# Kernel tuning notes

Measured on AMD Instinct MI355X. Metric: run time of the kernel, lower is better.

Reference implementation:

```python
import jax, jax.numpy as jnp
import numpy as np

B, C, H, W = 8, 256, 64, 64
CI = 128  # inter_channels = in_channels // reduction

def _conv1x1(x, w, b):
    # x: [b, c, h, w], w: [o, c], b: [o]
    return jnp.einsum('bchw,oc->bohw', x, w) + b[None, :, None, None]

def setup_inputs() -> dict:
    key = jax.random.key(0)
    ks = jax.random.split(key, 5)
    s_in = 1.0 / np.sqrt(C)
    s_ci = 1.0 / np.sqrt(CI)
    return {
        'x': jax.random.normal(ks[0], (B, C, H, W), jnp.float32),
        'w_g': jax.random.normal(ks[1], (CI, C), jnp.float32) * s_in,
        'b_g': jnp.zeros((CI,), jnp.float32),
        'w_theta': jax.random.normal(ks[2], (CI, C), jnp.float32) * s_in,
        'b_theta': jnp.zeros((CI,), jnp.float32),
        'w_phi': jax.random.normal(ks[3], (CI, C), jnp.float32) * s_in,
        'b_phi': jnp.zeros((CI,), jnp.float32),
        'w_out': jax.random.normal(ks[4], (C, CI), jnp.float32) * s_ci,
        'b_out': jnp.zeros((C,), jnp.float32),
    }

def reference(x, w_g, b_g, w_theta, b_theta, w_phi, b_phi, w_out, b_out):
    n, c, h, w = x.shape
    N = h * w
    g_x = _conv1x1(x, w_g, b_g).reshape(n, CI, N).transpose(0, 2, 1)        # [b, N, ci]
    theta_x = _conv1x1(x, w_theta, b_theta).reshape(n, CI, N).transpose(0, 2, 1)  # [b, N, ci]
    phi_x = _conv1x1(x, w_phi, b_phi).reshape(n, CI, N)                     # [b, ci, N]
    pw = jnp.einsum('bnc,bcm->bnm', theta_x, phi_x)                         # [b, N, N]
    # Faithful to source: divides by ci**(-0.5) == multiplies by sqrt(ci)
    pw = pw / (jnp.asarray(CI, x.dtype) ** -0.5)
    pw = jax.nn.softmax(pw, axis=-1)
    y = jnp.einsum('bnm,bmc->bnc', pw, g_x)                                 # [b, N, ci]
    y = y.transpose(0, 2, 1).reshape(n, CI, h, w)
    return x + _conv1x1(y, w_out, b_out)
```

## Files before the change

### kernel.cpp

```cpp
#include <hip/hip_runtime.h>
#include <hip/hip_bf16.h>
#include <stdint.h>
#include <stddef.h>


typedef __bf16 bf16;
typedef __attribute__((ext_vector_type(8))) __bf16 bf16x8;
typedef __attribute__((ext_vector_type(4))) __bf16 bf16x4;
typedef __attribute__((ext_vector_type(4))) float  f32x4;
typedef __attribute__((ext_vector_type(4))) int    i32x4;

#define MFMA16(a, b, c) __builtin_amdgcn_mfma_f32_16x16x32_bf16((a), (b), (c), 0, 0, 0)

constexpr int NB  = 8;
constexpr int NC  = 256;
constexpr int NN  = 4096;
constexpr int NCI = 128;
constexpr size_t NEL = (size_t)NB * NN * NCI;
constexpr int PBATCH = NN * NCI;

#define QSCALE (11.313708498984761f * 1.4426950408889634f)


__global__ __launch_bounds__(256) void k_proj(
    const float* __restrict__ x,
    const float* __restrict__ wt, const float* __restrict__ bt,
    const float* __restrict__ wp, const float* __restrict__ bp,
    const float* __restrict__ wg, const float* __restrict__ bg,
    bf16* __restrict__ qh, bf16* __restrict__ ql,
    bf16* __restrict__ kh, bf16* __restrict__ kl,
    bf16* __restrict__ vv)
{
    const int nt  = blockIdx.x;
    const int pj  = blockIdx.y;
    const int b   = blockIdx.z;
    const int tid = threadIdx.x;
    const int wv  = tid >> 6;
    const int ln  = tid & 63;
    const int lg  = ln >> 4;
    const int lq  = ln & 15;

    const float* W;
    const float* bias;
    if (pj == 0)      { W = wt; bias = bt; }
    else if (pj == 1) { W = wp; bias = bp; }
    else              { W = wg; bias = bg; }
    const bool split = (pj != 2);

    __shared__ char lds[49152];
    char* Ah = lds;
    char* Al = lds + 8192;
    char* Wh = lds + 16384;
    char* Wl = lds + 32768;

    f32x4 acc[8];
#pragma unroll
    for (int j = 0; j < 8; ++j) acc[j] = f32x4{0.f, 0.f, 0.f, 0.f};

    const int n0 = nt * 64;

    for (int c0 = 0; c0 < NC; c0 += 64) {
        __syncthreads();
#pragma unroll
        for (int p = 0; p < 4; ++p) {
            int cc = p * 16 + (tid >> 4);
            int nn = (tid & 15) * 4;
            f32x4 xv = *(const f32x4*)(x + ((size_t)b * NC + (c0 + cc)) * NN + n0 + nn);
#pragma unroll
            for (int e = 0; e < 4; ++e) {
                float f = xv[e];
                bf16 hh = (bf16)f;
                int row = nn + e;
                int off = (row * 128 + cc * 2) ^ ((row & 7) << 4);
                *(bf16*)(Ah + off) = hh;
                *(bf16*)(Al + off) = (bf16)(f - (float)hh);
            }
        }
#pragma unroll
        for (int p = 0; p < 8; ++p) {
            int i  = p * 16 + (tid >> 4);
            int c4 = (tid & 15) * 4;
            f32x4 w4 = *(const f32x4*)(W + (size_t)i * NC + c0 + c4);
            bf16x4 hv, lv;
#pragma unroll
            for (int e = 0; e < 4; ++e) {
                bf16 hh = (bf16)w4[e];
                hv[e] = hh;
                lv[e] = (bf16)(w4[e] - (float)hh);
            }
            int off = (i * 128 + c4 * 2) ^ ((i & 7) << 4);
            *(bf16x4*)(Wh + off) = hv;
            if (split) *(bf16x4*)(Wl + off) = lv;
        }
        __syncthreads();
#pragma unroll
        for (int kk = 0; kk < 2; ++kk) {
            int row  = wv * 16 + lq;
            int koff = kk * 64 + lg * 16;
            int aoff = (row * 128 + koff) ^ ((row & 7) << 4);
            bf16x8 ah = *(const bf16x8*)(Ah + aoff);
            bf16x8 al = *(const bf16x8*)(Al + aoff);
#pragma unroll
            for (int j = 0; j < 8; ++j) {
                int ir   = j * 16 + lq;
                int woff = (ir * 128 + koff) ^ ((ir & 7) << 4);
                bf16x8 bh = *(const bf16x8*)(Wh + woff);
                acc[j] = MFMA16(ah, bh, acc[j]);
                if (split) {
                    bf16x8 bl = *(const bf16x8*)(Wl + woff);
                    acc[j] = MFMA16(ah, bl, acc[j]);
                    acc[j] = MFMA16(al, bh, acc[j]);
                }
            }
        }
    }

    if (pj == 2) {
        __syncthreads();
        char* T = lds;
#pragma unroll
        for (int j = 0; j < 8; ++j) {
            int i = j * 16 + lq;
            float bv2 = bias[i];
#pragma unroll
            for (int r = 0; r < 4; ++r) {
                int nl = wv * 16 + lg * 4 + r;
                int off = (i * 128 + nl * 2) ^ ((i & 7) << 4);
                *(bf16*)(T + off) = (bf16)(acc[j][r] + bv2);
            }
        }
        __syncthreads();
#pragma unroll
        for (int p = 0; p < 4; ++p) {
            int i  = p * 32 + (tid >> 3);
            int sl = tid & 7;
            i32x4 tv = *(const i32x4*)(T + ((i * 128 + sl * 16) ^ ((i & 7) << 4)));
            size_t off = (size_t)b * PBATCH
                       + (size_t)((((nt * 8 + (i >> 4)) * 2 + (sl >> 2)) * 64
                                   + (sl & 3) * 16 + (i & 15)) * 8);
            *(i32x4*)(vv + off) = tv;
        }
    } else {
        const float sc = (pj == 0) ? QSCALE : 1.0f;
#pragma unroll
        for (int j = 0; j < 8; ++j) {
            int i = j * 16 + lq;
            float bv2 = bias[i];
#pragma unroll
            for (int r = 0; r < 4; ++r) {
                int q = n0 + wv * 16 + lg * 4 + r;
                size_t off = ((size_t)b * NN + q) * NCI + i;
                float val = (acc[j][r] + bv2) * sc;
                bf16 hh = (bf16)val;
                bf16 ll = (bf16)(val - (float)hh);
                if (pj == 0) { qh[off] = hh; ql[off] = ll; }
                else         { kh[off] = hh; kl[off] = ll; }
            }
        }
    }
}

__global__ __launch_bounds__(256, 2) void k_attn(
    const bf16* __restrict__ qh, const bf16* __restrict__ ql,
    const bf16* __restrict__ kh, const bf16* __restrict__ kl,
    const bf16* __restrict__ vf, bf16* __restrict__ y)
{
    const int bid = blockIdx.x;
    const int b   = bid & 7;
    const int qt  = bid >> 3;
    const int tid = threadIdx.x;
    const int wv  = tid >> 6;
    const int ln  = tid & 63;
    const int lg  = ln >> 4;
    const int lq  = ln & 15;
    const int n0  = qt * 64;

    __shared__ __attribute__((aligned(16))) char lds[40960];
    char* KH = lds;
    char* KL = lds + 16384;
    char* P  = lds + 32768 + wv * 2048;

    bf16x8 qhf[4], qlf[4];
    {
        int qrow = n0 + wv * 16 + lq;
        const bf16* bh = qh + ((size_t)b * NN + qrow) * NCI;
        const bf16* bl = ql + ((size_t)b * NN + qrow) * NCI;
#pragma unroll
        for (int kk = 0; kk < 4; ++kk) {
            int d0 = kk * 32 + lg * 8;
            qhf[kk] = *(const bf16x8*)(bh + d0);
            qlf[kk] = *(const bf16x8*)(bl + d0);
        }
    }

    f32x4 o[8];
#pragma unroll
    for (int j = 0; j < 8; ++j) o[j] = f32x4{0.f, 0.f, 0.f, 0.f};
    float mrun = -1e30f, lrun = 0.f;

    const bf16* vb = vf + (size_t)b * PBATCH + (size_t)ln * 8;

    for (int m0 = 0; m0 < NN; m0 += 64) {
        __syncthreads();
#pragma unroll
        for (int p = 0; p < 4; ++p) {
            int mm = p * 16 + (tid >> 4);
            int sl = tid & 15;
            size_t g = ((size_t)b * NN + m0 + mm) * NCI + sl * 8;
            int off = (mm * 256 + sl * 16) ^ ((mm & 7) << 4);
            *(i32x4*)(KH + off) = *(const i32x4*)(kh + g);
            *(i32x4*)(KL + off) = *(const i32x4*)(kl + g);
        }
        __syncthreads();

        bf16x8 bv[8][2];
        {
            const bf16* vp = vb + (size_t)(m0 >> 6) * 8192;
#pragma unroll
            for (int j = 0; j < 8; ++j) {
                bv[j][0] = *(const bf16x8*)(vp + (j * 2 + 0) * 512);
                bv[j][1] = *(const bf16x8*)(vp + (j * 2 + 1) * 512);
            }
        }

        f32x4 s[4];
        __builtin_amdgcn_s_setprio(1);
#pragma unroll
        for (int jm = 0; jm < 4; ++jm) {
            s[jm] = f32x4{0.f, 0.f, 0.f, 0.f};
            const int mrow = jm * 16 + lq;
            const int sw = (mrow & 7) << 4;
#pragma unroll
            for (int kk = 0; kk < 4; ++kk) {
                int aoff = (mrow * 256 + kk * 64 + lg * 16) ^ sw;
                bf16x8 ah = *(const bf16x8*)(KH + aoff);
                bf16x8 al = *(const bf16x8*)(KL + aoff);
                s[jm] = MFMA16(ah, qhf[kk], s[jm]);
                s[jm] = MFMA16(al, qhf[kk], s[jm]);
                s[jm] = MFMA16(ah, qlf[kk], s[jm]);
            }
        }
        __builtin_amdgcn_s_setprio(0);

        float tm = s[0][0];
#pragma unroll
        for (int jm = 0; jm < 4; ++jm)
#pragma unroll
            for (int r = 0; r < 4; ++r) tm = fmaxf(tm, s[jm][r]);
        tm = fmaxf(tm, __shfl_xor(tm, 16));
        tm = fmaxf(tm, __shfl_xor(tm, 32));

        if (__any(tm > mrun + 8.f)) {
            float mnew = fmaxf(mrun, tm);
            float alpha = exp2f(mrun - mnew);
            mrun = mnew;
            lrun *= alpha;
            float av[4];
#pragma unroll
            for (int r = 0; r < 4; ++r) av[r] = __shfl(alpha, lg * 4 + r);
#pragma unroll
            for (int j = 0; j < 8; ++j)
#pragma unroll
                for (int r = 0; r < 4; ++r) o[j][r] *= av[r];
        }

        float psum = 0.f;
#pragma unroll
        for (int jm = 0; jm < 4; ++jm) {
            bf16x4 pk;
#pragma unroll
            for (int r = 0; r < 4; ++r) {
                float e2 = exp2f(s[jm][r] - mrun);
                psum += e2;
                pk[r] = (bf16)e2;
            }
            int off = (lq * 128 + (jm * 16 + lg * 4) * 2) ^ ((lq & 7) << 4);
            *(bf16x4*)(P + off) = pk;
        }
        psum += __shfl_xor(psum, 16);
        psum += __shfl_xor(psum, 32);
        lrun += psum;

        bf16x8 pa[2];
#pragma unroll
        for (int tt = 0; tt < 2; ++tt)
            pa[tt] = *(const bf16x8*)(P + ((lq * 128 + tt * 64 + lg * 16) ^ ((lq & 7) << 4)));
        __builtin_amdgcn_s_setprio(1);
#pragma unroll
        for (int j = 0; j < 8; ++j) {
            o[j] = MFMA16(pa[0], bv[j][0], o[j]);
            o[j] = MFMA16(pa[1], bv[j][1], o[j]);
        }
        __builtin_amdgcn_s_setprio(0);
    }

    float rl[4];
#pragma unroll
    for (int r = 0; r < 4; ++r) rl[r] = 1.f / __shfl(lrun, lg * 4 + r);
#pragma unroll
    for (int j = 0; j < 8; ++j) {
        int d = j * 16 + lq;
#pragma unroll
        for (int r = 0; r < 4; ++r) {
            int q = n0 + wv * 16 + lg * 4 + r;
            y[((size_t)b * NN + q) * NCI + d] = (bf16)(o[j][r] * rl[r]);
        }
    }
}

__global__ __launch_bounds__(256) void k_out(
    const bf16* __restrict__ y, const float* __restrict__ x,
    const float* __restrict__ w_out, const float* __restrict__ b_out,
    float* __restrict__ out)
{
    const int nt  = blockIdx.x;
    const int b   = blockIdx.y;
    const int tid = threadIdx.x;
    const int wv  = tid >> 6;
    const int ln  = tid & 63;
    const int lg  = ln >> 4;
    const int lq  = ln & 15;
    const int n0  = nt * 64;

    __shared__ char Y[16384];
#pragma unroll
    for (int p = 0; p < 4; ++p) {
        int nn = p * 16 + (tid >> 4);
        int d0 = (tid & 15) * 8;
        i32x4 t = *(const i32x4*)(y + ((size_t)b * NN + n0 + nn) * NCI + d0);
        *(i32x4*)(Y + ((nn * 256 + d0 * 2) ^ ((nn & 7) << 4))) = t;
    }
    __syncthreads();

    bf16x8 af[4];
    {
        int row = wv * 16 + lq;
#pragma unroll
        for (int kk = 0; kk < 4; ++kk) {
            int koff = kk * 64 + lg * 16;
            af[kk] = *(const bf16x8*)(Y + ((row * 256 + koff) ^ ((row & 7) << 4)));
        }
    }

    f32x4 acc[16];
#pragma unroll
    for (int j = 0; j < 16; ++j) acc[j] = f32x4{0.f, 0.f, 0.f, 0.f};

#pragma unroll
    for (int j = 0; j < 16; ++j) {
        int c = j * 16 + lq;
#pragma unroll
        for (int kk = 0; kk < 4; ++kk) {
            int i0 = kk * 32 + lg * 8;
            f32x4 wa = *(const f32x4*)(w_out + (size_t)c * NCI + i0);
            f32x4 wb = *(const f32x4*)(w_out + (size_t)c * NCI + i0 + 4);
            bf16x8 bw;
#pragma unroll
            for (int e = 0; e < 4; ++e) { bw[e] = (bf16)wa[e]; bw[e + 4] = (bf16)wb[e]; }
            acc[j] = MFMA16(af[kk], bw, acc[j]);
        }
    }

#pragma unroll
    for (int j = 0; j < 16; ++j) {
        int c = j * 16 + lq;
        int nb = n0 + wv * 16 + lg * 4;
        size_t off = ((size_t)b * NC + c) * (size_t)NN + nb;
        f32x4 xv = *(const f32x4*)(x + off);
        float bo = b_out[c];
        f32x4 r;
#pragma unroll
        for (int t = 0; t < 4; ++t) r[t] = acc[j][t] + xv[t] + bo;
        *(f32x4*)(out + off) = r;
    }
}

extern "C" void kernel_launch(void* const* d_in, const int* in_sizes, int n_in,
                              void* d_out, int out_size, void* d_ws, size_t ws_size,
                              hipStream_t stream)
{
    (void)in_sizes; (void)n_in; (void)out_size; (void)ws_size;
    const float* x  = (const float*)d_in[0];
    const float* wg = (const float*)d_in[1];
    const float* bg = (const float*)d_in[2];
    const float* wt = (const float*)d_in[3];
    const float* bt = (const float*)d_in[4];
    const float* wp = (const float*)d_in[5];
    const float* bp = (const float*)d_in[6];
    const float* wo = (const float*)d_in[7];
    const float* bo = (const float*)d_in[8];
    float* out = (float*)d_out;

    char* ws = (char*)d_ws;
    bf16* qh = (bf16*)(ws);
    bf16* ql = (bf16*)(ws + NEL * 2);
    bf16* kh = (bf16*)(ws + NEL * 4);
    bf16* kl = (bf16*)(ws + NEL * 6);
    bf16* vv = (bf16*)(ws + NEL * 8);
    bf16* y  = qh;

    k_proj<<<dim3(64, 3, 8), 256, 0, stream>>>(x, wt, bt, wp, bp, wg, bg,
                                               qh, ql, kh, kl, vv);
    k_attn<<<dim3(512), 256, 0, stream>>>(qh, ql, kh, kl, vv, y);
    k_out<<<dim3(64, 8), 256, 0, stream>>>(y, x, wo, bo, out);
}
```

Measured before the change: 264.5 us.

## Double-buffer K tiles in LDS with register prefetch in attention loop

The attention kernel now keeps two LDS buffers for the K hi/lo tiles. The next tile's global loads are issued into registers before the current QK MFMAs and written to the other buffer afterwards, which leaves one barrier per iteration instead of two and hides global load latency behind compute. In exchange LDS grows from 40KB to 72KB per block, which may limit occupancy to fewer than the two blocks per CU requested by launch_bounds, and register pressure rises from the prefetch registers.

```diff
diff --git a/kernel.cpp b/kernel.cpp
--- a/kernel.cpp
+++ b/kernel.cpp
@@ -175,10 +175,11 @@
     const int lq  = ln & 15;
     const int n0  = qt * 64;
 
-    __shared__ __attribute__((aligned(16))) char lds[40960];
-    char* KH = lds;
-    char* KL = lds + 16384;
-    char* P  = lds + 32768 + wv * 2048;
+    __shared__ __attribute__((aligned(16))) char lds[73728];
+    char* P = lds + 65536 + wv * 2048;
+
+    const int smm = tid >> 4;
+    const int ssl = tid & 15;
 
     bf16x8 qhf[4], qlf[4];
     {
@@ -200,28 +201,47 @@
 
     const bf16* vb = vf + (size_t)b * PBATCH + (size_t)ln * 8;
 
-    for (int m0 = 0; m0 < NN; m0 += 64) {
-        __syncthreads();
+    {
 #pragma unroll
         for (int p = 0; p < 4; ++p) {
-            int mm = p * 16 + (tid >> 4);
-            int sl = tid & 15;
-            size_t g = ((size_t)b * NN + m0 + mm) * NCI + sl * 8;
-            int off = (mm * 256 + sl * 16) ^ ((mm & 7) << 4);
-            *(i32x4*)(KH + off) = *(const i32x4*)(kh + g);
-            *(i32x4*)(KL + off) = *(const i32x4*)(kl + g);
-        }
-        __syncthreads();
-
+            int mm = p * 16 + smm;
+            size_t g = ((size_t)b * NN + mm) * NCI + ssl * 8;
+            i32x4 hv = *(const i32x4*)(kh + g);
+            i32x4 lv = *(const i32x4*)(kl + g);
+            int off = (mm * 256 + ssl * 16) ^ ((mm & 7) << 4);
+            *(i32x4*)(lds + off) = hv;
+            *(i32x4*)(lds + 16384 + off) = lv;
+        }
+    }
+    __syncthreads();
+
+    for (int t = 0; t < 64; ++t) {
+        const int cur = t & 1;
+        char* KHc = lds + cur * 32768;
+        char* KLc = KHc + 16384;
+        char* KHn = lds + (cur ^ 1) * 32768;
+        char* KLn = KHn + 16384;
+        const bool pre = (t < 63);
+
+        i32x4 rkh[4], rkl[4];
+        if (pre) {
+#pragma unroll
+            for (int p = 0; p < 4; ++p) {
+                size_t g = ((size_t)b * NN + (t + 1) * 64 + p * 16 + smm) * NCI + ssl * 8;
+                rkh[p] = *(const i32x4*)(kh + g);
+                rkl[p] = *(const i32x4*)(kl + g);
+            }
+        }
         bf16x8 bv[8][2];
         {
-            const bf16* vp = vb + (size_t)(m0 >> 6) * 8192;
+            const bf16* vp = vb + (size_t)t * 8192;
 #pragma unroll
             for (int j = 0; j < 8; ++j) {
                 bv[j][0] = *(const bf16x8*)(vp + (j * 2 + 0) * 512);
                 bv[j][1] = *(const bf16x8*)(vp + (j * 2 + 1) * 512);
             }
         }
+        __builtin_amdgcn_sched_barrier(0);
 
         f32x4 s[4];
         __builtin_amdgcn_s_setprio(1);
@@ -233,14 +253,24 @@
 #pragma unroll
             for (int kk = 0; kk < 4; ++kk) {
                 int aoff = (mrow * 256 + kk * 64 + lg * 16) ^ sw;
-                bf16x8 ah = *(const bf16x8*)(KH + aoff);
-                bf16x8 al = *(const bf16x8*)(KL + aoff);
+                bf16x8 ah = *(const bf16x8*)(KHc + aoff);
+                bf16x8 al = *(const bf16x8*)(KLc + aoff);
                 s[jm] = MFMA16(ah, qhf[kk], s[jm]);
                 s[jm] = MFMA16(al, qhf[kk], s[jm]);
                 s[jm] = MFMA16(ah, qlf[kk], s[jm]);
             }
         }
         __builtin_amdgcn_s_setprio(0);
+
+        if (pre) {
+#pragma unroll
+            for (int p = 0; p < 4; ++p) {
+                int mm = p * 16 + smm;
+                int off = (mm * 256 + ssl * 16) ^ ((mm & 7) << 4);
+                *(i32x4*)(KHn + off) = rkh[p];
+                *(i32x4*)(KLn + off) = rkl[p];
+            }
+        }
 
         float tm = s[0][0];
 #pragma unroll
@@ -292,6 +322,8 @@
             o[j] = MFMA16(pa[1], bv[j][1], o[j]);
         }
         __builtin_amdgcn_s_setprio(0);
+
+        __syncthreads();
     }
 
     float rl[4];
```

Result: faster. 255.1 us (-3.5%).
